# Kernel optimization log

Hardware: AMD Instinct MI355X
Metric: run time of the kernel (lower is better)

## Reference

```python
import jax, jax.numpy as jnp
import numpy as np

V = 32000   # vocab.size
E = 512     # embed_dim
H = 512     # hidden_dim
L = 2       # num_layers
W = 32      # window_size
S = 512     # seq_len
B = 8       # batch


def setup_inputs() -> dict:
    key = jax.random.key(0)
    ks = jax.random.split(key, 2 + 4 * L)
    bound = 1.0 / np.sqrt(H)
    inp = {
        "encoder_input": jax.random.randint(ks[0], (S, B), 0, V),
        "embed_table": jax.random.normal(ks[1], (V, E), jnp.float32),
    }
    for l in range(L):
        in_dim = E if l == 0 else H
        k = ks[2 + 4 * l: 6 + 4 * l]
        inp[f"w_ih_{l}"] = jax.random.uniform(k[0], (4 * H, in_dim), jnp.float32, -bound, bound)
        inp[f"w_hh_{l}"] = jax.random.uniform(k[1], (4 * H, H), jnp.float32, -bound, bound)
        inp[f"b_ih_{l}"] = jax.random.uniform(k[2], (4 * H,), jnp.float32, -bound, bound)
        inp[f"b_hh_{l}"] = jax.random.uniform(k[3], (4 * H,), jnp.float32, -bound, bound)
    return inp


def _lstm_layer(x, mask, w_ih, w_hh, b_ih, b_hh):
    # x: [T, N, D]; mask: [T, N, 1]. Masked steps keep (h, c), so every window
    # effectively starts from a zero state at its first valid position (same as
    # running a fresh LSTM on each window, torch gate order i,f,g,o).
    N = x.shape[1]
    Hd = w_hh.shape[1]
    bias = b_ih + b_hh

    def step(carry, inp_):
        h, c = carry
        xt, mt = inp_
        gates = xt @ w_ih.T + h @ w_hh.T + bias  # [N, 4H]
        i, f, g, o = jnp.split(gates, 4, axis=-1)
        i = jax.nn.sigmoid(i)
        f = jax.nn.sigmoid(f)
        g = jnp.tanh(g)
        o = jax.nn.sigmoid(o)
        c_new = f * c + i * g
        h_new = o * jnp.tanh(c_new)
        h = jnp.where(mt, h_new, h)
        c = jnp.where(mt, c_new, c)
        return (h, c), h

    z = jnp.zeros((N, Hd), x.dtype)
    (h, _), ys = jax.lax.scan(step, (z, z), (x, mask))
    return ys, h


def reference(encoder_input, embed_table,
              w_ih_0, w_hh_0, b_ih_0, b_hh_0,
              w_ih_1, w_hh_1, b_ih_1, b_hh_1):
    emb = embed_table[encoder_input]              # [S, B, E]
    T = W + 1
    # window position t for target index i is i - W + t (invalid when < 0)
    pos = jnp.arange(S)[None, :] - W + jnp.arange(T)[:, None]  # [T, S]
    valid = pos >= 0
    windows = emb[jnp.clip(pos, 0)]               # [T, S, B, E]
    x = windows.reshape(T, S * B, E)
    mask = jnp.broadcast_to(valid[:, :, None], (T, S, B)).reshape(T, S * B, 1)

    params = [(w_ih_0, w_hh_0, b_ih_0, b_hh_0), (w_ih_1, w_hh_1, b_ih_1, b_hh_1)]
    h = None
    for (wi, wh, bi, bh) in params:
        x, h = _lstm_layer(x, mask, wi, wh, bi, bh)
    # original takes encoder_output at the last window position == final hidden
    return h.reshape(S, B, H)
```

## Files before the change

### kernel.cpp

```cpp
#include <hip/hip_runtime.h>
#include <stdint.h>

#define NROWS 4096
#define HDIM  512
#define GDIM  2048
#define WWIN  32

typedef __attribute__((ext_vector_type(8))) short short8;
typedef __attribute__((ext_vector_type(4))) float f32x4;

__device__ __forceinline__ unsigned short f2bf(float x){
  union { float f; unsigned int u; } v; v.f = x;
  unsigned int u = v.u + 0x7fffu + ((v.u >> 16) & 1u);
  return (unsigned short)(u >> 16);
}
__device__ __forceinline__ float bf2f(unsigned short u){
  union { unsigned int u; float f; } v; v.u = ((unsigned int)u) << 16; return v.f;
}

__device__ __forceinline__ void gld16(const void* g, void* l){
  __builtin_amdgcn_global_load_lds(
      (const __attribute__((address_space(1))) unsigned int*)g,
      (__attribute__((address_space(3))) unsigned int*)l, 16, 0, 0);
}

__device__ __forceinline__ float sigm(float x){ return 1.f/(1.f + __expf(-x)); }
__device__ __forceinline__ float tanh_f(float x){ return 1.f - 2.f/(1.f + __expf(2.f*x)); }

__device__ __forceinline__ void grid_sync(unsigned* bar, unsigned target){
  __syncthreads();
  if (threadIdx.x == 0){
    __builtin_amdgcn_fence(__ATOMIC_RELEASE, "agent");
    unsigned arrived = __hip_atomic_fetch_add(&bar[0], 1u, __ATOMIC_RELAXED,
                                              __HIP_MEMORY_SCOPE_AGENT);
    if (arrived == gridDim.x - 1){
      __hip_atomic_store(&bar[0], 0u, __ATOMIC_RELAXED, __HIP_MEMORY_SCOPE_AGENT);
      __hip_atomic_store(&bar[1], target, __ATOMIC_RELEASE, __HIP_MEMORY_SCOPE_AGENT);
    } else {
      while (__hip_atomic_load(&bar[1], __ATOMIC_RELAXED, __HIP_MEMORY_SCOPE_AGENT) < target)
        __builtin_amdgcn_s_sleep(8);
    }
    __builtin_amdgcn_fence(__ATOMIC_ACQUIRE, "agent");
  }
  __syncthreads();
}

__device__ __forceinline__ void gemm_tile_db(
    const char* A0, const char* A1, const char* Bsrc,
    int ldbB, int nk, int r0, int c0,
    char* smem, int wr, int wc, int lane, f32x4 acc[4][4])
{
  const int tid = threadIdx.x;
  const int oo0 = tid * 16;
  const int srow = oo0 >> 7;
  const int scb  = oo0 & 127;
  const size_t aOff = (size_t)(r0 + srow) * 1024 + scb;
  const size_t bOff = (size_t)(c0 + srow) * (size_t)ldbB + scb;

  auto STAGE = [&](int kk, int buf){
    const char* Ap = (kk < 8) ? A0 : A1;
    const size_t kbA = (size_t)(kk & 7) * 128;
    const size_t kbB = (size_t)kk * 128;
    char* AsB = smem + buf * 16384;
    char* BsB = smem + 32768 + buf * 16384;
    #pragma unroll
    for (int i = 0; i < 4; ++i){
      const size_t rstep = (size_t)i * 32;
      gld16(Ap   + aOff + rstep * 1024          + kbA, AsB + i*4096 + oo0);
      gld16(Bsrc + bOff + rstep * (size_t)ldbB  + kbB, BsB + i*4096 + oo0);
    }
  };

  STAGE(0, 0);
  __syncthreads();

  const int lr = lane & 15;
  const int lk = (lane >> 4) * 8;

  for (int kk = 0; kk < nk; ++kk){
    const int cur = kk & 1;
    if (kk + 1 < nk) STAGE(kk + 1, cur ^ 1);

    const unsigned short* As = (const unsigned short*)(smem + cur*16384);
    const unsigned short* Bs = (const unsigned short*)(smem + 32768 + cur*16384);
    short8 a[2][4], b[2][4];
    #pragma unroll
    for (int h = 0; h < 2; ++h){
      const int k32 = h * 32;
      #pragma unroll
      for (int m = 0; m < 4; ++m)
        a[h][m] = *(const short8*)(As + (64*wr + 16*m + lr)*64 + k32 + lk);
      #pragma unroll
      for (int n = 0; n < 4; ++n)
        b[h][n] = *(const short8*)(Bs + (64*wc + 16*n + lr)*64 + k32 + lk);
    }
    __builtin_amdgcn_s_setprio(1);
// ... 19 lines not shown
  const int j = blockIdx.x;
  const int g = j & 3, hd = j >> 2;
  const int r = g*512 + hd;
  for (int k = threadIdx.x; k < 512; k += 256){
    BrIh0[(size_t)j*512 + k]      = f2bf(wih0[(size_t)r*512 + k]);
    Br0  [(size_t)j*512 + k]      = f2bf(whh0[(size_t)r*512 + k]);
    Br1  [(size_t)j*1024 + k]     = f2bf(wih1[(size_t)r*512 + k]);
    Br1  [(size_t)j*1024 + 512+k] = f2bf(whh1[(size_t)r*512 + k]);
  }
  if (threadIdx.x == 0){
    bias0r[j] = bih0[r] + bhh0[r];
    br1[j]    = bih1[r] + bhh1[r];
  }
}

__global__ void __launch_bounds__(256) gather_embed(const int* enc, const float* tbl,
                                                    unsigned short* E)
{
  const int n = blockIdx.x;
  const int idx = enc[n];
  const float* src = tbl + (size_t)idx * 512;
  unsigned short* dst = E + (size_t)n * 512;
  for (int e = threadIdx.x; e < 512; e += 256) dst[e] = f2bf(src[e]);
}

__global__ void __launch_bounds__(256) p0_gemm(const unsigned short* E,
                                               const unsigned short* BrIh0,
                                               const float* bias0r,
                                               unsigned short* P0)
{
  __shared__ __align__(16) char smem[65536];
  const int tid  = threadIdx.x;
  const int lane = tid & 63, wid = tid >> 6;
  const int wr = wid >> 1, wc = wid & 1;
  const int bid = blockIdx.x;
  const int r0 = (bid >> 4) * 128, c0 = (bid & 15) * 128;
  f32x4 acc[4][4] = {};
  gemm_tile_db((const char*)E, nullptr, (const char*)BrIh0, 1024, 8,
               r0, c0, smem, wr, wc, lane, acc);
  #pragma unroll
  for (int m = 0; m < 4; ++m){
    const int rowb = r0 + 64*wr + 16*m + ((lane >> 4) << 2);
    #pragma unroll
    for (int n = 0; n < 4; ++n){
      const int colb = c0 + 64*wc + 16*n + (lane & 15);
      const float bs = bias0r[colb];
      #pragma unroll
      for (int r = 0; r < 4; ++r)
        P0[(size_t)(rowb + r)*GDIM + colb] = f2bf(acc[m][n][r] + bs);
    }
  }
}

__global__ void __launch_bounds__(512, 2) persist_kernel(
    unsigned short* h0, unsigned short* h1,
    const unsigned short* Br0, const unsigned short* Br1,
    const unsigned short* P0, const float* br1, float* out, unsigned* bar)
{
  extern __shared__ __align__(16) char smem[];

  const int x = blockIdx.x & 7, kq = blockIdx.x >> 3;
  const int wk = ((kq & 1) << 7) + x * 16 + (kq >> 1);
  const bool L1 = (wk >= 128);
  const int lb = L1 ? (wk - 128) : wk;
  const int r0  = (lb >> 3) * 256;
  const int c0v = (lb & 7) * 256;

  const int tid  = threadIdx.x;
  const int lane = tid & 63, wid = tid >> 6;
  const int wm = wid >> 2, wn = wid & 3;
  const int lr = lane & 15, sl = lane >> 4;

  const int srow  = tid >> 2;
  const int sbyte = ((tid & 3) ^ ((tid >> 3) & 3)) << 4;
  const int ph    = (sl ^ ((lr >> 1) & 3)) << 4;
  const int laneA = (wm*128 + lr) * 64 + ph;
  const int laneB = (wn*64  + lr) * 64 + ph;

  const char* Bp  = (const char*)(L1 ? Br1 : Br0);
  const int  ldbB = L1 ? 2048 : 1024;
  const int  nkt  = L1 ? 32 : 16;

  float creg[4][8];
  #pragma unroll
  for (int p = 0; p < 4; ++p)
    #pragma unroll
    for (int i = 0; i < 8; ++i) creg[p][i] = 0.f;

  for (int tau = 0; tau <= 33; ++tau){
    const bool active = L1 ? (tau >= 1) : (tau <= 32);
    if (active){
      const int t  = L1 ? (tau - 1) : tau;
      const int pr = (tau + 1) & 1, pw = tau & 1;
      const unsigned short* hA0 = h0 + (size_t)pr * (NROWS*HDIM);
      const unsigned short* hA1 = h1 + (size_t)pr * (NROWS*HDIM);

      auto STAGE_A = [&](int kt2, int c){
        const char* Ap; int kB;
        if (!L1 || kt2 < 16){ Ap = (const char*)hA0; kB = kt2 * 64; }
        else                { Ap = (const char*)hA1; kB = (kt2 - 16) * 64; }
        gld16(Ap + (size_t)(r0 + c*128 + srow) * 1024 + kB + sbyte,
              smem + (size_t)(kt2 & 3) * 32768 + c*8192 + tid*16);
      };
      auto STAGE_B = [&](int kt2, int c){
        gld16(Bp + (size_t)(c0v + c*128 + srow) * (size_t)ldbB + kt2*64 + sbyte,
              smem + (size_t)(kt2 & 3) * 32768 + 16384 + c*8192 + tid*16);
      };

      f32x4 acc[8][4] = {};

      STAGE_A(0,0); STAGE_A(0,1); STAGE_B(0,0); STAGE_B(0,1);
      STAGE_A(1,0); STAGE_A(1,1); STAGE_B(1,0); STAGE_B(1,1);
      asm volatile("s_waitcnt vmcnt(4)" ::: "memory");
      __builtin_amdgcn_s_barrier();

      for (int kt = 0; kt < nkt; ++kt){
        const char* bufp = smem + (size_t)(kt & 3) * 32768;
        const bool st = (kt + 2) < nkt;
        short8 a0[4], a1[4], b[4];

        #pragma unroll
        for (int m = 0; m < 4; ++m) a0[m] = *(const short8*)(bufp + laneA + m*1024);
        #pragma unroll
        for (int n = 0; n < 4; ++n) b[n]  = *(const short8*)(bufp + 16384 + laneB + n*1024);
        if (st){ STAGE_A(kt+2, 0); STAGE_A(kt+2, 1); }
        __builtin_amdgcn_s_barrier();
        asm volatile("s_waitcnt lgkmcnt(0)" ::: "memory");
        __builtin_amdgcn_sched_barrier(0);
        __builtin_amdgcn_s_setprio(1);
        #pragma unroll
        for (int m = 0; m < 4; ++m)
          #pragma unroll
          for (int n = 0; n < 4; ++n)
            acc[m][n] = __builtin_amdgcn_mfma_f32_16x16x32_bf16(a0[m], b[n], acc[m][n], 0, 0, 0);
        __builtin_amdgcn_s_setprio(0);
        __builtin_amdgcn_s_barrier();

        #pragma unroll
        for (int m = 0; m < 4; ++m) a1[m] = *(const short8*)(bufp + laneA + (4+m)*1024);
        if (st){
          STAGE_B(kt+2, 0); STAGE_B(kt+2, 1);
          asm volatile("s_waitcnt vmcnt(4)" ::: "memory");
        } else {
          asm volatile("s_waitcnt vmcnt(0)" ::: "memory");
        }
        __builtin_amdgcn_s_barrier();
        asm volatile("s_waitcnt lgkmcnt(0)" ::: "memory");
        __builtin_amdgcn_sched_barrier(0);
        __builtin_amdgcn_s_setprio(1);
        #pragma unroll
        for (int m = 0; m < 4; ++m)
          #pragma unroll
          for (int n = 0; n < 4; ++n)
            acc[4+m][n] = __builtin_amdgcn_mfma_f32_16x16x32_bf16(a1[m], b[n], acc[4+m][n], 0, 0, 0);
        __builtin_amdgcn_s_setprio(0);
        __builtin_amdgcn_s_barrier();
      }

      float* GLDS = (float*)smem;
      const int GST = 68;
      unsigned short* hw = (L1 ? h1 : h0) + (size_t)pw * (NROWS*HDIM);
      const bool finalStep = (L1 && t == 32);

      #pragma unroll
      for (int pass = 0; pass < 4; ++pass){
        __syncthreads();
        if (wn == pass){
          #pragma unroll
          for (int m = 0; m < 8; ++m){
            const int rowb = wm*128 + m*16 + (sl << 2);
            #pragma unroll
            for (int n = 0; n < 4; ++n){
              const int colb = n*16 + lr;
              const f32x4 v = acc[m][n];
              #pragma unroll
              for (int r = 0; r < 4; ++r)
                GLDS[(rowb + r)*GST + colb] = v[r];
            }
          }
        }
        __syncthreads();
        #pragma unroll
        for (int it = 0; it < 8; ++it){
          const int cid = it*512 + tid;
          const int row = cid >> 4;
          const int l   = cid & 15;
          const int rowg = r0 + row;
          const int hd   = (c0v >> 2) + pass*16 + l;
          float4 gv = *(const float4*)&GLDS[row*GST + 4*l];
          float gi = gv.x, gf = gv.y, gg = gv.z, go = gv.w;
          const int s  = rowg >> 3;
          const int bb = rowg & 7;
          const int pos = s - WWIN + t;
          if (!L1){
            const int p0r = (pos < 0 ? 0 : pos)*8 + bb;
            const ushort4 pv = *(const ushort4*)&P0[(size_t)p0r*GDIM + 4*hd];
            gi += bf2f(pv.x); gf += bf2f(pv.y); gg += bf2f(pv.z); go += bf2f(pv.w);
          } else {
            float4 bv = *(const float4*)&br1[4*hd];
            gi += bv.x; gf += bv.y; gg += bv.z; go += bv.w;
          }
          float cp = creg[pass][it];
          float i_ = sigm(gi), f_ = sigm(gf), g_ = tanh_f(gg), o_ = sigm(go);
          float cn = f_*cp + i_*g_;
          float hn = o_*tanh_f(cn);
          if (pos < 0){ cn = 0.f; hn = 0.f; }
          creg[pass][it] = cn;
          const size_t sidx = (size_t)rowg*HDIM + hd;
          if (finalStep) out[sidx] = hn;
          else           hw[sidx]  = f2bf(hn);
        }
      }
    }
    grid_sync(bar, (unsigned)(tau + 1));
  }
}

__global__ void __launch_bounds__(512, 2) step_kernel(
    unsigned short* h0, unsigned short* h1, float* c0b, float* c1b,
    const unsigned short* Br0, const unsigned short* Br1,
    const unsigned short* P0, const float* br1, float* out, int tau, int bidOff)
{
  extern __shared__ __align__(16) char smem[];

  const int x = blockIdx.x & 7, kq = blockIdx.x >> 3;
  int wk;
  if (gridDim.x == 256) wk = ((kq & 1) << 7) + x * 16 + (kq >> 1);
  else                  wk = x * 16 + kq;
  wk += bidOff;

  const bool L1 = (wk >= 128);
  const int t  = L1 ? (tau - 1) : tau;
  const int pr = (tau + 1) & 1, pw = tau & 1;
  const int lb = L1 ? (wk - 128) : wk;
  const int r0  = (lb >> 3) * 256;
  const int c0v = (lb & 7) * 256;

  const int tid  = threadIdx.x;
  const int lane = tid & 63;
  const int wid  = tid >> 6;
  const int wm = wid >> 2, wn = wid & 3;
  const int lr = lane & 15, sl = lane >> 4;

  const unsigned short* hA0 = h0 + (size_t)pr * (NROWS*HDIM);
  const unsigned short* hA1 = h1 + (size_t)pr * (NROWS*HDIM);
  const char* Bp  = (const char*)(L1 ? Br1 : Br0);
  const int  ldbB = L1 ? 2048 : 1024;
  const int  nkt  = L1 ? 32 : 16;

  const int srow  = tid >> 2;
  const int sbyte = ((tid & 3) ^ ((tid >> 3) & 3)) << 4;
  const int ph    = (sl ^ ((lr >> 1) & 3)) << 4;
  const int laneA = (wm*128 + lr) * 64 + ph;
  const int laneB = (wn*64  + lr) * 64 + ph;

  auto STAGE_A = [&](int kt2, int c){
    const char* Ap; int kB;
    if (!L1 || kt2 < 16){ Ap = (const char*)hA0; kB = kt2 * 64; }
    else                { Ap = (const char*)hA1; kB = (kt2 - 16) * 64; }
    gld16(Ap + (size_t)(r0 + c*128 + srow) * 1024 + kB + sbyte,
          smem + (size_t)(kt2 & 3) * 32768 + c*8192 + tid*16);
  };
  auto STAGE_B = [&](int kt2, int c){
    gld16(Bp + (size_t)(c0v + c*128 + srow) * (size_t)ldbB + kt2*64 + sbyte,
          smem + (size_t)(kt2 & 3) * 32768 + 16384 + c*8192 + tid*16);
  };

// ... 85 lines not shown
      if (!L1){
        const int p0r = (pos < 0 ? 0 : pos)*8 + bb;
        const ushort4 pv = *(const ushort4*)&P0[(size_t)p0r*GDIM + 4*hd];
        gi += bf2f(pv.x); gf += bf2f(pv.y); gg += bf2f(pv.z); go += bf2f(pv.w);
      } else {
        float4 bv = *(const float4*)&br1[4*hd];
        gi += bv.x; gf += bv.y; gg += bv.z; go += bv.w;
      }
      const size_t sidx = (size_t)rowg*HDIM + hd;
      float cp = cbuf[sidx];
      float i_ = sigm(gi), f_ = sigm(gf), g_ = tanh_f(gg), o_ = sigm(go);
      float cn = f_*cp + i_*g_;
      float hn = o_*tanh_f(cn);
      if (pos < 0){ cn = 0.f; hn = 0.f; }
      cbuf[sidx] = cn;
      if (finalStep) out[sidx] = hn;
      else           hw[sidx]  = f2bf(hn);
    }
  }
}

extern "C" void kernel_launch(void* const* d_in, const int* in_sizes, int n_in,
                              void* d_out, int out_size, void* d_ws, size_t ws_size,
                              hipStream_t stream)
{
  const int*   enc  = (const int*)d_in[0];
  const float* tbl  = (const float*)d_in[1];
  const float* wih0 = (const float*)d_in[2];
  const float* whh0 = (const float*)d_in[3];
  const float* bih0 = (const float*)d_in[4];
  const float* bhh0 = (const float*)d_in[5];
  const float* wih1 = (const float*)d_in[6];
  const float* whh1 = (const float*)d_in[7];
  const float* bih1 = (const float*)d_in[8];
  const float* bhh1 = (const float*)d_in[9];
  float* out = (float*)d_out;

  char* ws = (char*)d_ws;
  size_t off = 0;
  auto alloc = [&](size_t bytes){
    char* p = ws + off; off += (bytes + 255) & ~(size_t)255; return p;
  };
  unsigned short* E     = (unsigned short*)alloc((size_t)NROWS*512*2);
  unsigned short* BrIh0 = (unsigned short*)alloc((size_t)GDIM*512*2);
  unsigned short* Br0   = (unsigned short*)alloc((size_t)GDIM*512*2);
  unsigned short* Br1   = (unsigned short*)alloc((size_t)GDIM*1024*2);
  float* bias0r = (float*)alloc(GDIM*4);
  float* br1    = (float*)alloc(GDIM*4);
  unsigned short* P0 = (unsigned short*)alloc((size_t)NROWS*GDIM*2);
  unsigned short* h0 = (unsigned short*)alloc((size_t)2*NROWS*HDIM*2);
  unsigned short* h1 = (unsigned short*)alloc((size_t)2*NROWS*HDIM*2);
  float* c0 = (float*)alloc((size_t)NROWS*HDIM*4);
  float* c1 = (float*)alloc((size_t)NROWS*HDIM*4);
  unsigned* bar = (unsigned*)alloc(256);
  if (off > ws_size) return;

  (void)hipFuncSetAttribute(reinterpret_cast<const void*>(persist_kernel),
                            hipFuncAttributeMaxDynamicSharedMemorySize, 131072);
  (void)hipFuncSetAttribute(reinterpret_cast<const void*>(step_kernel),
                            hipFuncAttributeMaxDynamicSharedMemorySize, 131072);

  hipMemsetAsync(h0, 0, (size_t)33554688, stream);

  prep_weights<<<2048, 256, 0, stream>>>(wih0, whh0, bih0, bhh0,
                                         wih1, whh1, bih1, bhh1,
                                         BrIh0, Br0, Br1, bias0r, br1);
  gather_embed<<<4096, 256, 0, stream>>>(enc, tbl, E);
  p0_gemm<<<512, 256, 0, stream>>>(E, BrIh0, bias0r, P0);

  int occ = 0;
  hipError_t oe = hipOccupancyMaxActiveBlocksPerMultiprocessor(
      &occ, reinterpret_cast<const void*>(persist_kernel), 512, 131072);
  bool coop = (oe == hipSuccess && occ >= 1);
  if (coop){
    void* kargs[] = {&h0, &h1, &Br0, &Br1, &P0, &br1, &out, &bar};
    hipError_t le = hipLaunchCooperativeKernel(
        reinterpret_cast<const void*>(persist_kernel),
        dim3(256), dim3(512), kargs, 131072, stream);
    if (le != hipSuccess) coop = false;
  }
  if (!coop){
    for (int tau = 0; tau <= 33; ++tau){
      const int grid = (tau == 0 || tau == 33) ? 128 : 256;
      const int boff = (tau == 33) ? 128 : 0;
      step_kernel<<<grid, 512, 131072, stream>>>(h0, h1, c0, c1, Br0, Br1,
                                                 P0, br1, out, tau, boff);
    }
  }
}
```

Before: 1.741 ms.

## Drop grid-barrier fences, use relaxed atomic h traffic, restructure persistent GEMM pipeline

```diff
diff --git a/kernel.cpp b/kernel.cpp
--- a/kernel.cpp
+++ b/kernel.cpp
@@ -30,18 +30,17 @@
 __device__ __forceinline__ void grid_sync(unsigned* bar, unsigned target){
   __syncthreads();
   if (threadIdx.x == 0){
-    __builtin_amdgcn_fence(__ATOMIC_RELEASE, "agent");
     unsigned arrived = __hip_atomic_fetch_add(&bar[0], 1u, __ATOMIC_RELAXED,
                                               __HIP_MEMORY_SCOPE_AGENT);
     if (arrived == gridDim.x - 1){
       __hip_atomic_store(&bar[0], 0u, __ATOMIC_RELAXED, __HIP_MEMORY_SCOPE_AGENT);
-      __hip_atomic_store(&bar[1], target, __ATOMIC_RELEASE, __HIP_MEMORY_SCOPE_AGENT);
+      __hip_atomic_store(&bar[1], target, __ATOMIC_RELAXED, __HIP_MEMORY_SCOPE_AGENT);
     } else {
       while (__hip_atomic_load(&bar[1], __ATOMIC_RELAXED, __HIP_MEMORY_SCOPE_AGENT) < target)
         __builtin_amdgcn_s_sleep(8);
     }
-    __builtin_amdgcn_fence(__ATOMIC_ACQUIRE, "agent");
-  }
+  }
+  asm volatile("" ::: "memory");
   __syncthreads();
 }
 
@@ -174,33 +173,35 @@
 {
   extern __shared__ __align__(16) char smem[];
 
-  const int x = blockIdx.x & 7, kq = blockIdx.x >> 3;
-  const int wk = ((kq & 1) << 7) + x * 16 + (kq >> 1);
-  const bool L1 = (wk >= 128);
-  const int lb = L1 ? (wk - 128) : wk;
-  const int r0  = (lb >> 3) * 256;
-  const int c0v = (lb & 7) * 256;
+  const int bid = blockIdx.x;
+  const int x = bid & 7, i = bid >> 3;
+  const bool L1 = (i & 1);
+  const int rowg = (x >> 1) * 4 + ((i >> 1) & 3);
+  const int colg = (x & 1) * 4 + ((i >> 3) & 3);
+  const int r0  = rowg * 256;
+  const int c0v = colg * 256;
 
   const int tid  = threadIdx.x;
   const int lane = tid & 63, wid = tid >> 6;
   const int wm = wid >> 2, wn = wid & 3;
   const int lr = lane & 15, sl = lane >> 4;
-
-  const int srow  = tid >> 2;
-  const int sbyte = ((tid & 3) ^ ((tid >> 3) & 3)) << 4;
-  const int ph    = (sl ^ ((lr >> 1) & 3)) << 4;
-  const int laneA = (wm*128 + lr) * 64 + ph;
-  const int laneB = (wn*64  + lr) * 64 + ph;
+  const int ph = (sl ^ ((lr >> 1) & 3)) << 4;
+
+  const int srowB  = tid >> 2;
+  const int sbyteB = ((tid & 3) ^ ((tid >> 3) & 3)) << 4;
+  const int ar   = tid >> 1;
+  const int as0  = (tid & 1) * 2;
+  const int akey = (ar >> 1) & 3;
 
   const char* Bp  = (const char*)(L1 ? Br1 : Br0);
   const int  ldbB = L1 ? 2048 : 1024;
   const int  nkt  = L1 ? 32 : 16;
 
-  float creg[4][8];
+  float creg[4][4][2];
   #pragma unroll
   for (int p = 0; p < 4; ++p)
     #pragma unroll
-    for (int i = 0; i < 8; ++i) creg[p][i] = 0.f;
+    for (int q = 0; q < 4; ++q){ creg[p][q][0] = 0.f; creg[p][q][1] = 0.f; }
 
   for (int tau = 0; tau <= 33; ++tau){
     const bool active = L1 ? (tau >= 1) : (tau <= 32);
@@ -210,65 +211,73 @@
       const unsigned short* hA0 = h0 + (size_t)pr * (NROWS*HDIM);
       const unsigned short* hA1 = h1 + (size_t)pr * (NROWS*HDIM);
 
-      auto STAGE_A = [&](int kt2, int c){
-        const char* Ap; int kB;
-        if (!L1 || kt2 < 16){ Ap = (const char*)hA0; kB = kt2 * 64; }
-        else                { Ap = (const char*)hA1; kB = (kt2 - 16) * 64; }
-        gld16(Ap + (size_t)(r0 + c*128 + srow) * 1024 + kB + sbyte,
-              smem + (size_t)(kt2 & 3) * 32768 + c*8192 + tid*16);
+      auto issueB = [&](int kt2){
+        const char* s0 = Bp + (size_t)(c0v + srowB) * (size_t)ldbB + kt2*64 + sbyteB;
+        char* d = smem + 32768 + (size_t)(kt2 & 3) * 16384 + tid * 16;
+        gld16(s0, d);
+        gld16(s0 + (size_t)128 * (size_t)ldbB, d + 8192);
       };
-      auto STAGE_B = [&](int kt2, int c){
-        gld16(Bp + (size_t)(c0v + c*128 + srow) * (size_t)ldbB + kt2*64 + sbyte,
-              smem + (size_t)(kt2 & 3) * 32768 + 16384 + c*8192 + tid*16);
+      auto issueA = [&](int kt2, unsigned long long a[4]){
+        const unsigned short* hs; int kE;
+        if (!L1 || kt2 < 16){ hs = hA0; kE = kt2 * 32; }
+        else                { hs = hA1; kE = (kt2 - 16) * 32; }
+        unsigned long long* p = (unsigned long long*)(hs + (size_t)(r0 + ar) * 512 + kE + as0 * 8);
+        a[0] = __hip_atomic_load(p+0, __ATOMIC_RELAXED, __HIP_MEMORY_SCOPE_AGENT);
+        a[1] = __hip_atomic_load(p+1, __ATOMIC_RELAXED, __HIP_MEMORY_SCOPE_AGENT);
+        a[2] = __hip_atomic_load(p+2, __ATOMIC_RELAXED, __HIP_MEMORY_SCOPE_AGENT);
+        a[3] = __hip_atomic_load(p+3, __ATOMIC_RELAXED, __HIP_MEMORY_SCOPE_AGENT);
       };
+      auto writeA = [&](int kt2, const unsigned long long a[4]){
+        char* base = smem + (size_t)(kt2 & 1) * 16384 + ar * 64;
+        char* p0 = base + ((as0 ^ akey) << 4);
+        char* p1 = base + (((as0 + 1) ^ akey) << 4);
+        *(unsigned long long*)(p0)     = a[0];
+        *(unsigned long long*)(p0 + 8) = a[1];
+        *(unsigned long long*)(p1)     = a[2];
+        *(unsigned long long*)(p1 + 8) = a[3];
+      };
 
       f32x4 acc[8][4] = {};
-
-      STAGE_A(0,0); STAGE_A(0,1); STAGE_B(0,0); STAGE_B(0,1);
-      STAGE_A(1,0); STAGE_A(1,1); STAGE_B(1,0); STAGE_B(1,1);
+      unsigned long long areg[4];
+
+      issueA(0, areg);
+      issueB(0); issueB(1);
       asm volatile("s_waitcnt vmcnt(4)" ::: "memory");
+      writeA(0, areg);
+      issueA(1, areg);
+      asm volatile("s_waitcnt vmcnt(4)" ::: "memory");
+      asm volatile("s_waitcnt lgkmcnt(0)" ::: "memory");
       __builtin_amdgcn_s_barrier();
 
       for (int kt = 0; kt < nkt; ++kt){
-        const char* bufp = smem + (size_t)(kt & 3) * 32768;
-        const bool st = (kt + 2) < nkt;
-        short8 a0[4], a1[4], b[4];
-
+        const char* Ab = smem + (size_t)(kt & 1) * 16384;
+        const char* Bb = smem + 32768 + (size_t)(kt & 3) * 16384;
+        short8 a[8], b[4];
         #pragma unroll
-        for (int m = 0; m < 4; ++m) a0[m] = *(const short8*)(bufp + laneA + m*1024);
+        for (int m = 0; m < 8; ++m)
+          a[m] = *(const short8*)(Ab + (wm*128 + m*16 + lr)*64 + ph);
         #pragma unroll
-        for (int n = 0; n < 4; ++n) b[n]  = *(const short8*)(bufp + 16384 + laneB + n*1024);
-        if (st){ STAGE_A(kt+2, 0); STAGE_A(kt+2, 1); }
-        __builtin_amdgcn_s_barrier();
-        asm volatile("s_waitcnt lgkmcnt(0)" ::: "memory");
-        __builtin_amdgcn_sched_barrier(0);
+        for (int n = 0; n < 4; ++n)
+          b[n] = *(const short8*)(Bb + (wn*64 + n*16 + lr)*64 + ph);
+
+        const bool stB = (kt + 2) < nkt;
+        if (stB) issueB(kt + 2);
+
         __builtin_amdgcn_s_setprio(1);
         #pragma unroll
-        for (int m = 0; m < 4; ++m)
+        for (int m = 0; m < 8; ++m)
           #pragma unroll
           for (int n = 0; n < 4; ++n)
-            acc[m][n] = __builtin_amdgcn_mfma_f32_16x16x32_bf16(a0[m], b[n], acc[m][n], 0, 0, 0);
+            acc[m][n] = __builtin_amdgcn_mfma_f32_16x16x32_bf16(a[m], b[n], acc[m][n], 0, 0, 0);
         __builtin_amdgcn_s_setprio(0);
-        __builtin_amdgcn_s_barrier();
-
-        #pragma unroll
-        for (int m = 0; m < 4; ++m) a1[m] = *(const short8*)(bufp + laneA + (4+m)*1024);
-        if (st){
-          STAGE_B(kt+2, 0); STAGE_B(kt+2, 1);
-          asm volatile("s_waitcnt vmcnt(4)" ::: "memory");
-        } else {
-          asm volatile("s_waitcnt vmcnt(0)" ::: "memory");
+
+        if (stB) asm volatile("s_waitcnt vmcnt(2)" ::: "memory");
+        else     asm volatile("s_waitcnt vmcnt(0)" ::: "memory");
+        if (kt + 1 < nkt){
+          writeA(kt + 1, areg);
+          if (kt + 2 < nkt) issueA(kt + 2, areg);
         }
-        __builtin_amdgcn_s_barrier();
         asm volatile("s_waitcnt lgkmcnt(0)" ::: "memory");
-        __builtin_amdgcn_sched_barrier(0);
-        __builtin_amdgcn_s_setprio(1);
-        #pragma unroll
-        for (int m = 0; m < 4; ++m)
-          #pragma unroll
-          for (int n = 0; n < 4; ++n)
-            acc[4+m][n] = __builtin_amdgcn_mfma_f32_16x16x32_bf16(a1[m], b[n], acc[4+m][n], 0, 0, 0);
-        __builtin_amdgcn_s_setprio(0);
         __builtin_amdgcn_s_barrier();
       }
 
@@ -276,6 +285,7 @@
       const int GST = 68;
       unsigned short* hw = (L1 ? h1 : h0) + (size_t)pw * (NROWS*HDIM);
       const bool finalStep = (L1 && t == 32);
+      const int cbase = c0v >> 2;
 
       #pragma unroll
       for (int pass = 0; pass < 4; ++pass){
@@ -296,38 +306,60 @@
         }
         __syncthreads();
         #pragma unroll
-        for (int it = 0; it < 8; ++it){
-          const int cid = it*512 + tid;
-          const int row = cid >> 4;
-          const int l   = cid & 15;
+        for (int it = 0; it < 4; ++it){
+          const int pid = it*512 + tid;
+          const int row = pid >> 3;
+          const int pl  = (pid & 7) * 2;
           const int rowg = r0 + row;
-          const int hd   = (c0v >> 2) + pass*16 + l;
-          float4 gv = *(const float4*)&GLDS[row*GST + 4*l];
-          float gi = gv.x, gf = gv.y, gg = gv.z, go = gv.w;
+          const int hd0  = cbase + pass*16 + pl;
+          const float* gp = &GLDS[row*GST + 4*pl];
+          const float4 g0 = *(const float4*)gp;
+          const float4 g1 = *(const float4*)(gp + 4);
+          float gi0 = g0.x, gf0 = g0.y, gg0 = g0.z, go0 = g0.w;
+          float gi1 = g1.x, gf1 = g1.y, gg1 = g1.z, go1 = g1.w;
           const int s  = rowg >> 3;
           const int bb = rowg & 7;
           const int pos = s - WWIN + t;
           if (!L1){
             const int p0r = (pos < 0 ? 0 : pos)*8 + bb;
-            const ushort4 pv = *(const ushort4*)&P0[(size_t)p0r*GDIM + 4*hd];
-            gi += bf2f(pv.x); gf += bf2f(pv.y); gg += bf2f(pv.z); go += bf2f(pv.w);
+            const uint4 pv = *(const uint4*)&P0[(size_t)p0r*GDIM + 4*hd0];
+            gi0 += bf2f((unsigned short)(pv.x & 0xffff));
+            gf0 += bf2f((unsigned short)(pv.x >> 16));
+            gg0 += bf2f((unsigned short)(pv.y & 0xffff));
+            go0 += bf2f((unsigned short)(pv.y >> 16));
+            gi1 += bf2f((unsigned short)(pv.z & 0xffff));
+            gf1 += bf2f((unsigned short)(pv.z >> 16));
+            gg1 += bf2f((unsigned short)(pv.w & 0xffff));
+            go1 += bf2f((unsigned short)(pv.w >> 16));
           } else {
-            float4 bv = *(const float4*)&br1[4*hd];
-            gi += bv.x; gf += bv.y; gg += bv.z; go += bv.w;
+            const float4 b0 = *(const float4*)&br1[4*hd0];
+            const float4 b1 = *(const float4*)&br1[4*hd0 + 4];
+            gi0 += b0.x; gf0 += b0.y; gg0 += b0.z; go0 += b0.w;
+            gi1 += b1.x; gf1 += b1.y; gg1 += b1.z; go1 += b1.w;
           }
-          float cp = creg[pass][it];
-          float i_ = sigm(gi), f_ = sigm(gf), g_ = tanh_f(gg), o_ = sigm(go);
-          float cn = f_*cp + i_*g_;
-          float hn = o_*tanh_f(cn);
-          if (pos < 0){ cn = 0.f; hn = 0.f; }
-          creg[pass][it] = cn;
-          const size_t sidx = (size_t)rowg*HDIM + hd;
-          if (finalStep) out[sidx] = hn;
-          else           hw[sidx]  = f2bf(hn);
+          float cp0 = creg[pass][it][0];
+          float cp1 = creg[pass][it][1];
+          float i0 = sigm(gi0), f0 = sigm(gf0), gA = tanh_f(gg0), o0 = sigm(go0);
+          float i1 = sigm(gi1), f1 = sigm(gf1), gB = tanh_f(gg1), o1 = sigm(go1);
+          float cn0 = f0*cp0 + i0*gA;
+          float cn1 = f1*cp1 + i1*gB;
+          float hn0 = o0*tanh_f(cn0);
+          float hn1 = o1*tanh_f(cn1);
+          if (pos < 0){ cn0 = 0.f; hn0 = 0.f; cn1 = 0.f; hn1 = 0.f; }
+          creg[pass][it][0] = cn0;
+          creg[pass][it][1] = cn1;
+          const size_t sidx0 = (size_t)rowg*HDIM + hd0;
+          if (finalStep){
+            *(float2*)&out[sidx0] = make_float2(hn0, hn1);
+          } else {
+            const unsigned hp = (unsigned)f2bf(hn0) | ((unsigned)f2bf(hn1) << 16);
+            __hip_atomic_store((unsigned*)&hw[sidx0], hp, __ATOMIC_RELAXED,
+                               __HIP_MEMORY_SCOPE_AGENT);
+          }
         }
       }
     }
-    grid_sync(bar, (unsigned)(tau + 1));
+    if (tau != 33) grid_sync(bar, (unsigned)(tau + 1));
   }
 }
 
@@ -523,7 +555,7 @@
   if (off > ws_size) return;
 
   (void)hipFuncSetAttribute(reinterpret_cast<const void*>(persist_kernel),
-                            hipFuncAttributeMaxDynamicSharedMemorySize, 131072);
+                            hipFuncAttributeMaxDynamicSharedMemorySize, 98304);
   (void)hipFuncSetAttribute(reinterpret_cast<const void*>(step_kernel),
                             hipFuncAttributeMaxDynamicSharedMemorySize, 131072);
 
@@ -537,13 +569,13 @@
 
   int occ = 0;
   hipError_t oe = hipOccupancyMaxActiveBlocksPerMultiprocessor(
-      &occ, reinterpret_cast<const void*>(persist_kernel), 512, 131072);
+      &occ, reinterpret_cast<const void*>(persist_kernel), 512, 98304);
   bool coop = (oe == hipSuccess && occ >= 1);
   if (coop){
     void* kargs[] = {&h0, &h1, &Br0, &Br1, &P0, &br1, &out, &bar};
     hipError_t le = hipLaunchCooperativeKernel(
         reinterpret_cast<const void*>(persist_kernel),
-        dim3(256), dim3(512), kargs, 131072, stream);
+        dim3(256), dim3(512), kargs, 98304, stream);
     if (le != hipSuccess) coop = false;
   }
   if (!coop){
```

Result: no change. 1.739 ms (-0.1%).

## Replace grid barrier with per-XCC band sync and register-staged coherent A loads

Applied to the files above, without the earlier changes.

```diff
diff --git a/kernel.cpp b/kernel.cpp
--- a/kernel.cpp
+++ b/kernel.cpp
@@ -8,6 +8,7 @@
 
 typedef __attribute__((ext_vector_type(8))) short short8;
 typedef __attribute__((ext_vector_type(4))) float f32x4;
+typedef __attribute__((ext_vector_type(2))) unsigned long long u64x2;
 
 __device__ __forceinline__ unsigned short f2bf(float x){
   union { float f; unsigned int u; } v; v.f = x;
@@ -24,24 +25,24 @@
       (__attribute__((address_space(3))) unsigned int*)l, 16, 0, 0);
 }
 
+__device__ __forceinline__ unsigned long long ld_sc0_b64(const void* p){
+  unsigned long long r;
+  asm volatile("global_load_dwordx2 %0, %1, off sc0"
+               : "=v"(r) : "v"(p) : "memory");
+  return r;
+}
+
 __device__ __forceinline__ float sigm(float x){ return 1.f/(1.f + __expf(-x)); }
 __device__ __forceinline__ float tanh_f(float x){ return 1.f - 2.f/(1.f + __expf(2.f*x)); }
 
-__device__ __forceinline__ void grid_sync(unsigned* bar, unsigned target){
+__device__ __forceinline__ void band_sync(unsigned* ctr, unsigned target){
   __syncthreads();
   if (threadIdx.x == 0){
-    __builtin_amdgcn_fence(__ATOMIC_RELEASE, "agent");
-    unsigned arrived = __hip_atomic_fetch_add(&bar[0], 1u, __ATOMIC_RELAXED,
-                                              __HIP_MEMORY_SCOPE_AGENT);
-    if (arrived == gridDim.x - 1){
-      __hip_atomic_store(&bar[0], 0u, __ATOMIC_RELAXED, __HIP_MEMORY_SCOPE_AGENT);
-      __hip_atomic_store(&bar[1], target, __ATOMIC_RELEASE, __HIP_MEMORY_SCOPE_AGENT);
-    } else {
-      while (__hip_atomic_load(&bar[1], __ATOMIC_RELAXED, __HIP_MEMORY_SCOPE_AGENT) < target)
-        __builtin_amdgcn_s_sleep(8);
-    }
-    __builtin_amdgcn_fence(__ATOMIC_ACQUIRE, "agent");
-  }
+    __hip_atomic_fetch_add(ctr, 1u, __ATOMIC_RELAXED, __HIP_MEMORY_SCOPE_AGENT);
+    while (__hip_atomic_load(ctr, __ATOMIC_RELAXED, __HIP_MEMORY_SCOPE_AGENT) < target)
+      __builtin_amdgcn_s_sleep(2);
+  }
+  asm volatile("" ::: "memory");
   __syncthreads();
 }
 
@@ -167,40 +168,59 @@
   }
 }
 
-__global__ void __launch_bounds__(512, 2) persist_kernel(
+__global__ void __launch_bounds__(512, 1) persist_kernel(
     unsigned short* h0, unsigned short* h1,
     const unsigned short* Br0, const unsigned short* Br1,
     const unsigned short* P0, const float* br1, float* out, unsigned* bar)
 {
   extern __shared__ __align__(16) char smem[];
-
-  const int x = blockIdx.x & 7, kq = blockIdx.x >> 3;
-  const int wk = ((kq & 1) << 7) + x * 16 + (kq >> 1);
-  const bool L1 = (wk >= 128);
-  const int lb = L1 ? (wk - 128) : wk;
-  const int r0  = (lb >> 3) * 256;
-  const int c0v = (lb & 7) * 256;
+  __shared__ int role_s;
 
   const int tid  = threadIdx.x;
+  if (tid == 0){
+    unsigned xcc;
+    asm volatile("s_getreg_b32 %0, hwreg(HW_REG_XCC_ID)" : "=s"(xcc));
+    xcc &= 7u;
+    unsigned slot = __hip_atomic_fetch_add(&bar[xcc * 32], 1u, __ATOMIC_RELAXED,
+                                           __HIP_MEMORY_SCOPE_AGENT);
+    role_s = (int)((xcc << 5) | (slot & 31u));
+  }
+  __syncthreads();
+  const int role = role_s;
+  const int xcc = role >> 5, j = role & 31;
+  const bool L1 = (j & 1);
+  const int sub  = (j >> 1) & 1;
+  const int colg = j >> 2;
+  const int r0   = xcc * 512 + sub * 256;
+  const int c0v  = colg * 256;
+
   const int lane = tid & 63, wid = tid >> 6;
   const int wm = wid >> 2, wn = wid & 3;
   const int lr = lane & 15, sl = lane >> 4;
-
-  const int srow  = tid >> 2;
-  const int sbyte = ((tid & 3) ^ ((tid >> 3) & 3)) << 4;
-  const int ph    = (sl ^ ((lr >> 1) & 3)) << 4;
+  const int ph = (sl ^ ((lr >> 1) & 3)) << 4;
   const int laneA = (wm*128 + lr) * 64 + ph;
   const int laneB = (wn*64  + lr) * 64 + ph;
+
+  const int ar   = tid >> 1;
+  const int s0   = (tid & 1) * 2;
+  const int akey = (ar >> 1) & 3;
+  const int off0 = ar*64 + ((s0 ^ akey) << 4);
+  const int off1 = ar*64 + (((s0 + 1) ^ akey) << 4);
+
+  const int srowB  = tid >> 2;
+  const int sbyteB = ((tid & 3) ^ ((tid >> 3) & 3)) << 4;
 
   const char* Bp  = (const char*)(L1 ? Br1 : Br0);
   const int  ldbB = L1 ? 2048 : 1024;
   const int  nkt  = L1 ? 32 : 16;
 
+  unsigned* ctr = bar + 512 + xcc * 32;
+
   float creg[4][8];
   #pragma unroll
   for (int p = 0; p < 4; ++p)
     #pragma unroll
-    for (int i = 0; i < 8; ++i) creg[p][i] = 0.f;
+    for (int q = 0; q < 8; ++q) creg[p][q] = 0.f;
 
   for (int tau = 0; tau <= 33; ++tau){
     const bool active = L1 ? (tau >= 1) : (tau <= 32);
@@ -210,65 +230,80 @@
       const unsigned short* hA0 = h0 + (size_t)pr * (NROWS*HDIM);
       const unsigned short* hA1 = h1 + (size_t)pr * (NROWS*HDIM);
 
-      auto STAGE_A = [&](int kt2, int c){
-        const char* Ap; int kB;
-        if (!L1 || kt2 < 16){ Ap = (const char*)hA0; kB = kt2 * 64; }
-        else                { Ap = (const char*)hA1; kB = (kt2 - 16) * 64; }
-        gld16(Ap + (size_t)(r0 + c*128 + srow) * 1024 + kB + sbyte,
-              smem + (size_t)(kt2 & 3) * 32768 + c*8192 + tid*16);
+      unsigned long long A0r, A1r, A2r, A3r;
+      auto issueA = [&](int kt2){
+        const unsigned short* hs; int kB;
+        if (!L1 || kt2 < 16){ hs = hA0; kB = kt2 * 64; }
+        else                { hs = hA1; kB = (kt2 - 16) * 64; }
+        const char* base = (const char*)hs + (size_t)(r0 + ar) * 1024 + kB + s0*16;
+        A0r = ld_sc0_b64(base);
+        A1r = ld_sc0_b64(base + 8);
+        A2r = ld_sc0_b64(base + 16);
+        A3r = ld_sc0_b64(base + 24);
       };
-      auto STAGE_B = [&](int kt2, int c){
-        gld16(Bp + (size_t)(c0v + c*128 + srow) * (size_t)ldbB + kt2*64 + sbyte,
-              smem + (size_t)(kt2 & 3) * 32768 + 16384 + c*8192 + tid*16);
+      auto writeA = [&](int kt2){
+        char* Ab = smem + (size_t)(kt2 & 1) * 16384;
+        u64x2 v0; v0[0] = A0r; v0[1] = A1r;
+        u64x2 v1; v1[0] = A2r; v1[1] = A3r;
+        *(u64x2*)(Ab + off0) = v0;
+        *(u64x2*)(Ab + off1) = v1;
       };
+      auto issueB = [&](int kt2){
+        char* d = smem + 32768 + (size_t)(kt2 & 1) * 16384 + tid * 16;
+        #pragma unroll
+        for (int c = 0; c < 2; ++c)
+          gld16(Bp + (size_t)(c0v + c*128 + srowB) * (size_t)ldbB + kt2*64 + sbyteB,
+                d + c*8192);
+      };
 
       f32x4 acc[8][4] = {};
 
-      STAGE_A(0,0); STAGE_A(0,1); STAGE_B(0,0); STAGE_B(0,1);
-      STAGE_A(1,0); STAGE_A(1,1); STAGE_B(1,0); STAGE_B(1,1);
+      issueA(0);
+      asm volatile("s_waitcnt vmcnt(0)" ::: "memory");
+      __builtin_amdgcn_sched_barrier(0);
+      writeA(0);
+      issueB(0);
+      issueA(1);
       asm volatile("s_waitcnt vmcnt(4)" ::: "memory");
+      asm volatile("s_waitcnt lgkmcnt(0)" ::: "memory");
       __builtin_amdgcn_s_barrier();
 
       for (int kt = 0; kt < nkt; ++kt){
-        const char* bufp = smem + (size_t)(kt & 3) * 32768;
-        const bool st = (kt + 2) < nkt;
-        short8 a0[4], a1[4], b[4];
-
-        #pragma unroll
-        for (int m = 0; m < 4; ++m) a0[m] = *(const short8*)(bufp + laneA + m*1024);
-        #pragma unroll
-        for (int n = 0; n < 4; ++n) b[n]  = *(const short8*)(bufp + 16384 + laneB + n*1024);
-        if (st){ STAGE_A(kt+2, 0); STAGE_A(kt+2, 1); }
-        __builtin_amdgcn_s_barrier();
-        asm volatile("s_waitcnt lgkmcnt(0)" ::: "memory");
-        __builtin_amdgcn_sched_barrier(0);
+        const bool n1 = (kt + 1) < nkt, n2 = (kt + 2) < nkt;
+        if (n1) issueB(kt + 1);
+
+        const char* Ab = smem + (size_t)(kt & 1) * 16384;
+        const char* Bb = smem + 32768 + (size_t)(kt & 1) * 16384;
+        short8 a[8], b[4];
+        #pragma unroll
+        for (int m = 0; m < 8; ++m)
+          a[m] = *(const short8*)(Ab + laneA + m*1024);
+        #pragma unroll
+        for (int n = 0; n < 4; ++n)
+          b[n] = *(const short8*)(Bb + laneB + n*1024);
+
         __builtin_amdgcn_s_setprio(1);
         #pragma unroll
-        for (int m = 0; m < 4; ++m)
+        for (int m = 0; m < 8; ++m)
           #pragma unroll
           for (int n = 0; n < 4; ++n)
-            acc[m][n] = __builtin_amdgcn_mfma_f32_16x16x32_bf16(a0[m], b[n], acc[m][n], 0, 0, 0);
+            acc[m][n] = __builtin_amdgcn_mfma_f32_16x16x32_bf16(a[m], b[n], acc[m][n], 0, 0, 0);
         __builtin_amdgcn_s_setprio(0);
-        __builtin_amdgcn_s_barrier();
-
-        #pragma unroll
-        for (int m = 0; m < 4; ++m) a1[m] = *(const short8*)(bufp + laneA + (4+m)*1024);
-        if (st){
-          STAGE_B(kt+2, 0); STAGE_B(kt+2, 1);
-          asm volatile("s_waitcnt vmcnt(4)" ::: "memory");
+
+        if (n1){
+          asm volatile("s_waitcnt vmcnt(2)" ::: "memory");
+          __builtin_amdgcn_sched_barrier(0);
+          writeA(kt + 1);
+          if (n2){
+            issueA(kt + 2);
+            asm volatile("s_waitcnt vmcnt(4)" ::: "memory");
+          } else {
+            asm volatile("s_waitcnt vmcnt(0)" ::: "memory");
+          }
         } else {
           asm volatile("s_waitcnt vmcnt(0)" ::: "memory");
         }
-        __builtin_amdgcn_s_barrier();
         asm volatile("s_waitcnt lgkmcnt(0)" ::: "memory");
-        __builtin_amdgcn_sched_barrier(0);
-        __builtin_amdgcn_s_setprio(1);
-        #pragma unroll
-        for (int m = 0; m < 4; ++m)
-          #pragma unroll
-          for (int n = 0; n < 4; ++n)
-            acc[4+m][n] = __builtin_amdgcn_mfma_f32_16x16x32_bf16(a1[m], b[n], acc[4+m][n], 0, 0, 0);
-        __builtin_amdgcn_s_setprio(0);
         __builtin_amdgcn_s_barrier();
       }
 
@@ -276,6 +311,7 @@
       const int GST = 68;
       unsigned short* hw = (L1 ? h1 : h0) + (size_t)pw * (NROWS*HDIM);
       const bool finalStep = (L1 && t == 32);
+      const int cbase = c0v >> 2;
 
       #pragma unroll
       for (int pass = 0; pass < 4; ++pass){
@@ -301,12 +337,12 @@
           const int row = cid >> 4;
           const int l   = cid & 15;
           const int rowg = r0 + row;
-          const int hd   = (c0v >> 2) + pass*16 + l;
+          const int hd   = cbase + pass*16 + l;
           float4 gv = *(const float4*)&GLDS[row*GST + 4*l];
           float gi = gv.x, gf = gv.y, gg = gv.z, go = gv.w;
-          const int s  = rowg >> 3;
+          const int sI = rowg >> 3;
           const int bb = rowg & 7;
-          const int pos = s - WWIN + t;
+          const int pos = sI - WWIN + t;
           if (!L1){
             const int p0r = (pos < 0 ? 0 : pos)*8 + bb;
             const ushort4 pv = *(const ushort4*)&P0[(size_t)p0r*GDIM + 4*hd];
@@ -327,7 +363,7 @@
         }
       }
     }
-    grid_sync(bar, (unsigned)(tau + 1));
+    if (tau != 33) band_sync(ctr, 32u * (unsigned)(tau + 1));
   }
 }
 
@@ -519,15 +555,15 @@
   unsigned short* h1 = (unsigned short*)alloc((size_t)2*NROWS*HDIM*2);
   float* c0 = (float*)alloc((size_t)NROWS*HDIM*4);
   float* c1 = (float*)alloc((size_t)NROWS*HDIM*4);
-  unsigned* bar = (unsigned*)alloc(256);
+  unsigned* bar = (unsigned*)alloc(8192);
   if (off > ws_size) return;
 
   (void)hipFuncSetAttribute(reinterpret_cast<const void*>(persist_kernel),
-                            hipFuncAttributeMaxDynamicSharedMemorySize, 131072);
+                            hipFuncAttributeMaxDynamicSharedMemorySize, 98304);
   (void)hipFuncSetAttribute(reinterpret_cast<const void*>(step_kernel),
                             hipFuncAttributeMaxDynamicSharedMemorySize, 131072);
 
-  hipMemsetAsync(h0, 0, (size_t)33554688, stream);
+  hipMemsetAsync(h0, 0, (size_t)33562624, stream);
 
   prep_weights<<<2048, 256, 0, stream>>>(wih0, whh0, bih0, bhh0,
                                          wih1, whh1, bih1, bhh1,
@@ -537,13 +573,13 @@
 
   int occ = 0;
   hipError_t oe = hipOccupancyMaxActiveBlocksPerMultiprocessor(
-      &occ, reinterpret_cast<const void*>(persist_kernel), 512, 131072);
+      &occ, reinterpret_cast<const void*>(persist_kernel), 512, 98304);
   bool coop = (oe == hipSuccess && occ >= 1);
   if (coop){
     void* kargs[] = {&h0, &h1, &Br0, &Br1, &P0, &br1, &out, &bar};
     hipError_t le = hipLaunchCooperativeKernel(
         reinterpret_cast<const void*>(persist_kernel),
-        dim3(256), dim3(512), kargs, 131072, stream);
+        dim3(256), dim3(512), kargs, 98304, stream);
     if (le != hipSuccess) coop = false;
   }
   if (!coop){
```

New measurement: 1.741 ms. About the same (-0.0%).

## Replace grid-wide barrier with per-XCC band sync and XCC-local row tiling

Applied to the files above, without the earlier changes.

```diff
diff --git a/kernel.cpp b/kernel.cpp
--- a/kernel.cpp
+++ b/kernel.cpp
@@ -27,21 +27,14 @@
 __device__ __forceinline__ float sigm(float x){ return 1.f/(1.f + __expf(-x)); }
 __device__ __forceinline__ float tanh_f(float x){ return 1.f - 2.f/(1.f + __expf(2.f*x)); }
 
-__device__ __forceinline__ void grid_sync(unsigned* bar, unsigned target){
+__device__ __forceinline__ void band_sync(unsigned* ctr, unsigned target){
   __syncthreads();
   if (threadIdx.x == 0){
-    __builtin_amdgcn_fence(__ATOMIC_RELEASE, "agent");
-    unsigned arrived = __hip_atomic_fetch_add(&bar[0], 1u, __ATOMIC_RELAXED,
-                                              __HIP_MEMORY_SCOPE_AGENT);
-    if (arrived == gridDim.x - 1){
-      __hip_atomic_store(&bar[0], 0u, __ATOMIC_RELAXED, __HIP_MEMORY_SCOPE_AGENT);
-      __hip_atomic_store(&bar[1], target, __ATOMIC_RELEASE, __HIP_MEMORY_SCOPE_AGENT);
-    } else {
-      while (__hip_atomic_load(&bar[1], __ATOMIC_RELAXED, __HIP_MEMORY_SCOPE_AGENT) < target)
-        __builtin_amdgcn_s_sleep(8);
-    }
-    __builtin_amdgcn_fence(__ATOMIC_ACQUIRE, "agent");
-  }
+    __hip_atomic_fetch_add(ctr, 1u, __ATOMIC_RELAXED, __HIP_MEMORY_SCOPE_AGENT);
+    while (__hip_atomic_load(ctr, __ATOMIC_RELAXED, __HIP_MEMORY_SCOPE_AGENT) < target)
+      __builtin_amdgcn_s_sleep(2);
+  }
+  asm volatile("" ::: "memory");
   __syncthreads();
 }
 
@@ -167,40 +160,52 @@
   }
 }
 
-__global__ void __launch_bounds__(512, 2) persist_kernel(
+__global__ void __launch_bounds__(256, 2) persist_kernel(
     unsigned short* h0, unsigned short* h1,
     const unsigned short* Br0, const unsigned short* Br1,
     const unsigned short* P0, const float* br1, float* out, unsigned* bar)
 {
   extern __shared__ __align__(16) char smem[];
-
-  const int x = blockIdx.x & 7, kq = blockIdx.x >> 3;
-  const int wk = ((kq & 1) << 7) + x * 16 + (kq >> 1);
-  const bool L1 = (wk >= 128);
-  const int lb = L1 ? (wk - 128) : wk;
-  const int r0  = (lb >> 3) * 256;
-  const int c0v = (lb & 7) * 256;
-
-  const int tid  = threadIdx.x;
-  const int lane = tid & 63, wid = tid >> 6;
-  const int wm = wid >> 2, wn = wid & 3;
+  __shared__ int role_s;
+
+  const int tid = threadIdx.x;
+  if (tid == 0){
+    unsigned xcc;
+    asm volatile("s_getreg_b32 %0, hwreg(HW_REG_XCC_ID)" : "=s"(xcc));
+    xcc &= 7u;
+    unsigned slot = __hip_atomic_fetch_add(&bar[xcc * 32], 1u, __ATOMIC_RELAXED,
+                                           __HIP_MEMORY_SCOPE_AGENT);
+    role_s = (int)((xcc << 6) | (slot & 63u));
+  }
+  __syncthreads();
+  const int role = role_s;
+  const int xcc = role >> 6, j = role & 63;
+  const bool L1 = (j & 1);
+  const int sub  = (j >> 1) & 3;
+  const int colg = j >> 3;
+  const int r0   = xcc * 512 + sub * 128;
+  const int c0v  = colg * 256;
+
+  const int lane = tid & 63, wn = tid >> 6;
   const int lr = lane & 15, sl = lane >> 4;
-
-  const int srow  = tid >> 2;
-  const int sbyte = ((tid & 3) ^ ((tid >> 3) & 3)) << 4;
-  const int ph    = (sl ^ ((lr >> 1) & 3)) << 4;
-  const int laneA = (wm*128 + lr) * 64 + ph;
-  const int laneB = (wn*64  + lr) * 64 + ph;
+  const int ph = (sl ^ ((lr >> 1) & 3)) << 4;
+  const int laneA = lr * 64 + ph;
+  const int laneB = (wn*64 + lr) * 64 + ph;
+
+  const int srowS = tid >> 2;
+  const int ls16  = ((tid & 3) ^ ((tid >> 3) & 3)) << 4;
 
   const char* Bp  = (const char*)(L1 ? Br1 : Br0);
   const int  ldbB = L1 ? 2048 : 1024;
   const int  nkt  = L1 ? 32 : 16;
 
+  unsigned* ctr = bar + 512 + xcc * 32;
+
   float creg[4][8];
   #pragma unroll
   for (int p = 0; p < 4; ++p)
     #pragma unroll
-    for (int i = 0; i < 8; ++i) creg[p][i] = 0.f;
+    for (int q = 0; q < 8; ++q) creg[p][q] = 0.f;
 
   for (int tau = 0; tau <= 33; ++tau){
     const bool active = L1 ? (tau >= 1) : (tau <= 32);
@@ -210,35 +215,41 @@
       const unsigned short* hA0 = h0 + (size_t)pr * (NROWS*HDIM);
       const unsigned short* hA1 = h1 + (size_t)pr * (NROWS*HDIM);
 
-      auto STAGE_A = [&](int kt2, int c){
-        const char* Ap; int kB;
-        if (!L1 || kt2 < 16){ Ap = (const char*)hA0; kB = kt2 * 64; }
-        else                { Ap = (const char*)hA1; kB = (kt2 - 16) * 64; }
-        gld16(Ap + (size_t)(r0 + c*128 + srow) * 1024 + kB + sbyte,
-              smem + (size_t)(kt2 & 3) * 32768 + c*8192 + tid*16);
+      auto STAGE_A = [&](int kt2){
+        char* d = smem + (size_t)(kt2 % 3) * 8192 + tid * 16;
+        const unsigned short* hs; int kB;
+        if (!L1 || kt2 < 16){ hs = hA0; kB = kt2 * 64; }
+        else                { hs = hA1; kB = (kt2 - 16) * 64; }
+        const char* s = (const char*)hs + (size_t)(r0 + srowS) * 1024 + kB + ls16;
+        gld16(s, d);
+        gld16(s + (size_t)64 * 1024, d + 4096);
       };
-      auto STAGE_B = [&](int kt2, int c){
-        gld16(Bp + (size_t)(c0v + c*128 + srow) * (size_t)ldbB + kt2*64 + sbyte,
-              smem + (size_t)(kt2 & 3) * 32768 + 16384 + c*8192 + tid*16);
+      auto STAGE_Bu = [&](int kt2, int u){
+        char* d = smem + 24576 + (size_t)(kt2 % 3) * 16384 + u * 8192 + tid * 16;
+        const char* s = Bp + (size_t)(c0v + u*128 + srowS) * (size_t)ldbB
+                           + kt2 * 64 + ls16;
+        gld16(s, d);
+        gld16(s + (size_t)64 * (size_t)ldbB, d + 4096);
       };
 
       f32x4 acc[8][4] = {};
 
-      STAGE_A(0,0); STAGE_A(0,1); STAGE_B(0,0); STAGE_B(0,1);
-      STAGE_A(1,0); STAGE_A(1,1); STAGE_B(1,0); STAGE_B(1,1);
-      asm volatile("s_waitcnt vmcnt(4)" ::: "memory");
+      STAGE_A(0); STAGE_Bu(0,0); STAGE_Bu(0,1);
+      STAGE_A(1); STAGE_Bu(1,0); STAGE_Bu(1,1);
+      asm volatile("s_waitcnt vmcnt(6)" ::: "memory");
       __builtin_amdgcn_s_barrier();
 
       for (int kt = 0; kt < nkt; ++kt){
-        const char* bufp = smem + (size_t)(kt & 3) * 32768;
+        const char* Ab = smem + (size_t)(kt % 3) * 8192;
+        const char* Bb = smem + 24576 + (size_t)(kt % 3) * 16384;
         const bool st = (kt + 2) < nkt;
-        short8 a0[4], a1[4], b[4];
-
-        #pragma unroll
-        for (int m = 0; m < 4; ++m) a0[m] = *(const short8*)(bufp + laneA + m*1024);
-        #pragma unroll
-        for (int n = 0; n < 4; ++n) b[n]  = *(const short8*)(bufp + 16384 + laneB + n*1024);
-        if (st){ STAGE_A(kt+2, 0); STAGE_A(kt+2, 1); }
+        short8 b[4], a0[4], a1[4];
+
+        #pragma unroll
+        for (int n = 0; n < 4; ++n) b[n]  = *(const short8*)(Bb + laneB + n*1024);
+        #pragma unroll
+        for (int m = 0; m < 4; ++m) a0[m] = *(const short8*)(Ab + laneA + m*1024);
+        if (st) STAGE_Bu(kt + 2, 0);
         __builtin_amdgcn_s_barrier();
         asm volatile("s_waitcnt lgkmcnt(0)" ::: "memory");
         __builtin_amdgcn_sched_barrier(0);
@@ -252,13 +263,8 @@
         __builtin_amdgcn_s_barrier();
 
         #pragma unroll
-        for (int m = 0; m < 4; ++m) a1[m] = *(const short8*)(bufp + laneA + (4+m)*1024);
-        if (st){
-          STAGE_B(kt+2, 0); STAGE_B(kt+2, 1);
-          asm volatile("s_waitcnt vmcnt(4)" ::: "memory");
-        } else {
-          asm volatile("s_waitcnt vmcnt(0)" ::: "memory");
-        }
+        for (int m = 0; m < 4; ++m) a1[m] = *(const short8*)(Ab + laneA + 4096 + m*1024);
+        if (st){ STAGE_Bu(kt + 2, 1); STAGE_A(kt + 2); }
         __builtin_amdgcn_s_barrier();
         asm volatile("s_waitcnt lgkmcnt(0)" ::: "memory");
         __builtin_amdgcn_sched_barrier(0);
@@ -269,6 +275,8 @@
           for (int n = 0; n < 4; ++n)
             acc[4+m][n] = __builtin_amdgcn_mfma_f32_16x16x32_bf16(a1[m], b[n], acc[4+m][n], 0, 0, 0);
         __builtin_amdgcn_s_setprio(0);
+        if (st) asm volatile("s_waitcnt vmcnt(6)" ::: "memory");
+        else    asm volatile("s_waitcnt vmcnt(0)" ::: "memory");
         __builtin_amdgcn_s_barrier();
       }
 
@@ -276,6 +284,7 @@
       const int GST = 68;
       unsigned short* hw = (L1 ? h1 : h0) + (size_t)pw * (NROWS*HDIM);
       const bool finalStep = (L1 && t == 32);
+      const int cbase = c0v >> 2;
 
       #pragma unroll
       for (int pass = 0; pass < 4; ++pass){
@@ -283,7 +292,7 @@
         if (wn == pass){
           #pragma unroll
           for (int m = 0; m < 8; ++m){
-            const int rowb = wm*128 + m*16 + (sl << 2);
+            const int rowb = m*16 + (sl << 2);
             #pragma unroll
             for (int n = 0; n < 4; ++n){
               const int colb = n*16 + lr;
@@ -297,16 +306,16 @@
         __syncthreads();
         #pragma unroll
         for (int it = 0; it < 8; ++it){
-          const int cid = it*512 + tid;
+          const int cid = it*256 + tid;
           const int row = cid >> 4;
           const int l   = cid & 15;
           const int rowg = r0 + row;
-          const int hd   = (c0v >> 2) + pass*16 + l;
+          const int hd   = cbase + pass*16 + l;
           float4 gv = *(const float4*)&GLDS[row*GST + 4*l];
           float gi = gv.x, gf = gv.y, gg = gv.z, go = gv.w;
-          const int s  = rowg >> 3;
+          const int sI = rowg >> 3;
           const int bb = rowg & 7;
-          const int pos = s - WWIN + t;
+          const int pos = sI - WWIN + t;
           if (!L1){
             const int p0r = (pos < 0 ? 0 : pos)*8 + bb;
             const ushort4 pv = *(const ushort4*)&P0[(size_t)p0r*GDIM + 4*hd];
@@ -327,7 +336,7 @@
         }
       }
     }
-    grid_sync(bar, (unsigned)(tau + 1));
+    if (tau != 33) band_sync(ctr, 64u * (unsigned)(tau + 1));
   }
 }
 
@@ -519,15 +528,15 @@
   unsigned short* h1 = (unsigned short*)alloc((size_t)2*NROWS*HDIM*2);
   float* c0 = (float*)alloc((size_t)NROWS*HDIM*4);
   float* c1 = (float*)alloc((size_t)NROWS*HDIM*4);
-  unsigned* bar = (unsigned*)alloc(256);
+  unsigned* bar = (unsigned*)alloc(8192);
   if (off > ws_size) return;
 
   (void)hipFuncSetAttribute(reinterpret_cast<const void*>(persist_kernel),
-                            hipFuncAttributeMaxDynamicSharedMemorySize, 131072);
+                            hipFuncAttributeMaxDynamicSharedMemorySize, 73728);
   (void)hipFuncSetAttribute(reinterpret_cast<const void*>(step_kernel),
                             hipFuncAttributeMaxDynamicSharedMemorySize, 131072);
 
-  hipMemsetAsync(h0, 0, (size_t)33554688, stream);
+  hipMemsetAsync(h0, 0, (size_t)33562624, stream);
 
   prep_weights<<<2048, 256, 0, stream>>>(wih0, whh0, bih0, bhh0,
                                          wih1, whh1, bih1, bhh1,
@@ -537,13 +546,13 @@
 
   int occ = 0;
   hipError_t oe = hipOccupancyMaxActiveBlocksPerMultiprocessor(
-      &occ, reinterpret_cast<const void*>(persist_kernel), 512, 131072);
-  bool coop = (oe == hipSuccess && occ >= 1);
+      &occ, reinterpret_cast<const void*>(persist_kernel), 256, 73728);
+  bool coop = (oe == hipSuccess && occ >= 2);
   if (coop){
     void* kargs[] = {&h0, &h1, &Br0, &Br1, &P0, &br1, &out, &bar};
     hipError_t le = hipLaunchCooperativeKernel(
         reinterpret_cast<const void*>(persist_kernel),
-        dim3(256), dim3(512), kargs, 131072, stream);
+        dim3(512), dim3(256), kargs, 73728, stream);
     if (le != hipSuccess) coop = false;
   }
   if (!coop){
```

After: 1.740 ms. About the same (-0.1%).
